# Kernel tuning notes

Measured on AMD Instinct MI355X. Metric: run time of the kernel, lower is better.

The kernel has to match this reference:

```python
import jax, jax.numpy as jnp
import numpy as np

# Module constants (from init_kwargs): 2D domain, m=[1024,1024], omega=[0,1,0,1]
PAD = 2
M0, M1 = 1024, 1024
OMEGA_LO = np.array([0.0, 0.0], dtype=np.float32)   # omega[0::2]
H = np.array([1.0 / 1024.0, 1.0 / 1024.0], dtype=np.float32)  # (omega_hi-omega_lo)/m
N_POINTS = 2097152


def _b0(j, xi):
    # Cubic B-spline basis pieces, exactly as SplineInter.b0
    if j == 1:
        return (2 + xi) * (2 + xi) * (2 + xi)
    elif j == 2:
        return -(3 * xi + 6) * (xi * xi) + 4
    elif j == 3:
        return (3 * xi - 6) * (xi * xi) + 4
    elif j == 4:
        return (2 - xi) * (2 - xi) * (2 - xi)


def _basis(t):
    # t: [N] fractional part; returns [N,4] weights for offsets j=-1,0,1,2
    # matches b0(3 - j, t - j)
    return jnp.stack([_b0(3 - j, t - j) for j in range(-1, 3)], axis=-1)


def setup_inputs() -> dict:
    key = jax.random.key(0)
    k1, k2 = jax.random.split(key)
    # query points in physical domain [0,1)^2 -> normalized coords in [-0.5, 1023.5)
    x = jax.random.uniform(k1, (N_POINTS, 2), dtype=jnp.float32)
    # padded spline coefficient grid: (M0+2*PAD, M1+2*PAD)
    coeffs = 0.1 * jax.random.normal(k2, (M0 + 2 * PAD, M1 + 2 * PAD), dtype=jnp.float32)
    return {"x": x, "coeffs": coeffs}


def reference(x, coeffs):
    x = x.reshape(-1, 2)
    # normalize to grid coords
    xn = (x - jnp.asarray(OMEGA_LO)) / jnp.asarray(H) - 0.5  # [N,2]
    m = jnp.array([M0, M1], dtype=xn.dtype)
    valid = jnp.all((xn > -2) & (xn < m), axis=1)            # [N]
    P = jnp.floor(xn).astype(jnp.int32)                      # [N,2]
    t = xn - P                                               # fractional part [N,2]

    i1 = M1 + 2 * PAD  # row stride of padded coeff grid
    p = i1 * (PAD + P[:, 0]) + (PAD + P[:, 1])               # [N] base flat index

    w0 = _basis(t[:, 0])  # [N,4]
    w1 = _basis(t[:, 1])  # [N,4]

    js = jnp.arange(-1, 3, dtype=jnp.int32)
    idx = p[:, None, None] + js[:, None] * i1 + js[None, :]  # [N,4,4]
    cflat = coeffs.reshape(-1)
    safe_idx = jnp.clip(idx, 0, cflat.shape[0] - 1)
    vals = cflat[safe_idx]                                   # [N,4,4] gathered stencil

    out = jnp.einsum('nij,ni,nj->n', vals, w0, w1)
    out = jnp.where(valid, out, 0.0)
    return out[:, None]  # [N,1]
```

## Files before the change

### kernel.cpp

```cpp
#include <hip/hip_runtime.h>


#define I1 1028
#define TOTAL (1028 * 1028)
#define NQR 257
#define QELEMS (NQR * I1)

typedef float f4u __attribute__((ext_vector_type(4), aligned(4)));

__device__ __forceinline__ void basis4(float t, float w[4]) {
    float a = 1.0f - t;
    w[0] = a * a * a;
    w[1] = (3.0f * t - 6.0f) * (t * t) + 4.0f;
    float xi = t - 1.0f;
    w[2] = -(3.0f * xi + 6.0f) * (xi * xi) + 4.0f;
    w[3] = t * t * t;
}

struct PointSetup {
    int base;
    int r0, c0;
    bool valid;
    bool qinterior;
    float w0[4], w1[4];
};

__device__ __forceinline__ PointSetup setup_point(float px, float py) {
    PointSetup ps;
    float xn0 = px * 1024.0f - 0.5f;
    float xn1 = py * 1024.0f - 0.5f;

    ps.valid = (xn0 > -2.0f) && (xn0 < 1024.0f) &&
               (xn1 > -2.0f) && (xn1 < 1024.0f);

    float P0f = floorf(xn0);
    float P1f = floorf(xn1);
    int P0 = (int)P0f;
    int P1 = (int)P1f;
    float t0 = xn0 - P0f;
    float t1 = xn1 - P1f;

    basis4(t0, ps.w0);
    basis4(t1, ps.w1);

    ps.base = I1 * (2 + P0) + (2 + P1);
    ps.r0 = P0 + 1;
    ps.c0 = P1 + 1;
    ps.qinterior = (ps.r0 >= 0) && (ps.r0 <= 1023) &&
                   (ps.c0 >= 0) && (ps.c0 + 3 <= 1027);
    return ps;
}

__device__ __forceinline__ float eval_slow(const float* __restrict__ coeffs,
                                           const PointSetup& ps) {
    float acc = 0.0f;
#pragma unroll
    for (int j = 0; j < 4; ++j) {
        int r = ps.base + (j - 1) * I1 - 1;
        float s = 0.0f;
#pragma unroll
        for (int k = 0; k < 4; ++k) {
            int idx = r + k;
            idx = min(max(idx, 0), TOTAL - 1);
            s = fmaf(coeffs[idx], ps.w1[k], s);
        }
        acc = fmaf(s, ps.w0[j], acc);
    }
    return acc;
}

__device__ __forceinline__ void shifted_w8(const float w0[4], int s, float W[8]) {
#pragma unroll
    for (int t = 0; t < 8; ++t) {
        float v = 0.0f;
        if (t - 0 >= 0 && t - 0 < 4) v = (s == 0) ? w0[t - 0] : v;
        if (t - 1 >= 0 && t - 1 < 4) v = (s == 1) ? w0[t - 1] : v;
        if (t - 2 >= 0 && t - 2 < 4) v = (s == 2) ? w0[t - 2] : v;
        if (t - 3 >= 0 && t - 3 < 4) v = (s == 3) ? w0[t - 3] : v;
        W[t] = v;
    }
}

__device__ __forceinline__ float reduce_quad(const float4 A[4], const float4 B[4],
                                             const float W[8], const float w1[4]) {
    float acc = 0.0f;
#pragma unroll
    for (int k = 0; k < 4; ++k) {
        float sk = fmaf(A[k].x, W[0],
                   fmaf(A[k].y, W[1],
                   fmaf(A[k].z, W[2],
                   fmaf(A[k].w, W[3],
                   fmaf(B[k].x, W[4],
                   fmaf(B[k].y, W[5],
                   fmaf(B[k].z, W[6],
                        B[k].w * W[7])))))));
        acc = fmaf(sk, w1[k], acc);
    }
    return acc;
}


__global__ __launch_bounds__(256) void quadpack_kernel(
    const float* __restrict__ coeffs, float4* __restrict__ Q)
{
    int i = blockIdx.x * blockDim.x + threadIdx.x;
    if (i >= QELEMS) return;
    int qr = i / I1;
    int c  = i - qr * I1;
    int r  = 4 * qr;
    float4 v;
    v.x = coeffs[(r + 0) * I1 + c];
    v.y = coeffs[(r + 1) * I1 + c];
    v.z = coeffs[(r + 2) * I1 + c];
    v.w = coeffs[(r + 3) * I1 + c];
    Q[i] = v;
}


__global__ __launch_bounds__(256) void eval_quad_kernel(
    const float* __restrict__ x,
    const float* __restrict__ coeffs,
    const float4* __restrict__ Q,
    float* __restrict__ out, int n)
{
    int g = blockIdx.x * blockDim.x + threadIdx.x;
    int i0 = 2 * g;
    if (i0 >= n) return;

    if (i0 + 1 < n) {
        float4 two = reinterpret_cast<const float4*>(x)[g];
        PointSetup psA = setup_point(two.x, two.y);
        PointSetup psB = setup_point(two.z, two.w);

        float accA, accB;
        if (psA.qinterior && psB.qinterior) {
            int sA = psA.r0 & 3, sB = psB.r0 & 3;
            const float4* qA = Q + (psA.r0 >> 2) * I1 + psA.c0;
            const float4* qB = Q + (psB.r0 >> 2) * I1 + psB.c0;
            float4 A0[4], A1[4], B0[4], B1[4];
#pragma unroll
            for (int k = 0; k < 4; ++k) {
                A0[k] = qA[k];
                B0[k] = qB[k];
            }
#pragma unroll
            for (int k = 0; k < 4; ++k) {
                A1[k] = qA[I1 + k];
                B1[k] = qB[I1 + k];
            }
            float WA[8], WB[8];
            shifted_w8(psA.w0, sA, WA);
            shifted_w8(psB.w0, sB, WB);
            accA = reduce_quad(A0, A1, WA, psA.w1);
            accB = reduce_quad(B0, B1, WB, psB.w1);
        } else {
            accA = eval_slow(coeffs, psA);
            accB = eval_slow(coeffs, psB);
        }

        float2 o;
        o.x = psA.valid ? accA : 0.0f;
        o.y = psB.valid ? accB : 0.0f;
        reinterpret_cast<float2*>(out)[g] = o;
    } else {
        float px = x[2 * i0], py = x[2 * i0 + 1];
        PointSetup ps = setup_point(px, py);
        float acc = eval_slow(coeffs, ps);
        out[i0] = ps.valid ? acc : 0.0f;
    }
}


__global__ __launch_bounds__(256) void spline_interp_kernel(
    const float* __restrict__ x,
    const float* __restrict__ coeffs,
    float* __restrict__ out,
    int n, int half)
{
    int i = blockIdx.x * blockDim.x + threadIdx.x;
    if (i >= half) return;
    int i2 = i + half;

    float2 xyA = reinterpret_cast<const float2*>(x)[i];
    float2 xyB = reinterpret_cast<const float2*>(x)[i2];

    PointSetup psA = setup_point(xyA.x, xyA.y);
    PointSetup psB = setup_point(xyB.x, xyB.y);

    float accA, accB;
    bool interiorA = (psA.base - I1 - 1 >= 0) && (psA.base + 2 * I1 + 2 <= TOTAL - 1);
    bool interiorB = (psB.base - I1 - 1 >= 0) && (psB.base + 2 * I1 + 2 <= TOTAL - 1);
    if (interiorA && interiorB) {
        f4u vA[4], vB[4];
#pragma unroll
        for (int j = 0; j < 4; ++j) {
            vA[j] = *reinterpret_cast<const f4u*>(coeffs + psA.base + (j - 1) * I1 - 1);
            vB[j] = *reinterpret_cast<const f4u*>(coeffs + psB.base + (j - 1) * I1 - 1);
        }
        float a0 = 0.0f, a1 = 0.0f;
#pragma unroll
        for (int j = 0; j < 4; ++j) {
            float s0 = fmaf(vA[j].x, psA.w1[0], fmaf(vA[j].y, psA.w1[1],
                       fmaf(vA[j].z, psA.w1[2], vA[j].w * psA.w1[3])));
            a0 = fmaf(s0, psA.w0[j], a0);
            float s1 = fmaf(vB[j].x, psB.w1[0], fmaf(vB[j].y, psB.w1[1],
                       fmaf(vB[j].z, psB.w1[2], vB[j].w * psB.w1[3])));
            a1 = fmaf(s1, psB.w0[j], a1);
        }
        accA = a0; accB = a1;
    } else {
        accA = eval_slow(coeffs, psA);
        accB = eval_slow(coeffs, psB);
    }

    out[i]  = psA.valid ? accA : 0.0f;
    out[i2] = psB.valid ? accB : 0.0f;
}


extern "C" void kernel_launch(void* const* d_in, const int* in_sizes, int n_in,
                              void* d_out, int out_size, void* d_ws, size_t ws_size,
                              hipStream_t stream) {
    const float* x = (const float*)d_in[0];
    const float* coeffs = (const float*)d_in[1];
    float* out = (float*)d_out;

    int n = in_sizes[0] / 2;

    size_t o_q  = 0;
    size_t need = (size_t)QELEMS * 16;

    if (ws_size >= need) {
        float4* Q = (float4*)((char*)d_ws + o_q);

        int gpack = (QELEMS + 255) / 256;
        quadpack_kernel<<<gpack, 256, 0, stream>>>(coeffs, Q);

        int pairs = (n + 1) / 2;
        int geval = (pairs + 255) / 256;
        eval_quad_kernel<<<geval, 256, 0, stream>>>(x, coeffs, Q, out, n);
    } else {
        int half = n / 2;
        int block = 256;
        int grid = (half + block - 1) / block;
        spline_interp_kernel<<<grid, block, 0, stream>>>(x, coeffs, out, n, half);
    }
}
```

Before: 107.0 us.

## Pack four row-phase-shifted float4 copies so each point reads one 4x4 stencil

Replaces the single 4-row-packed coefficient table with four copies, each starting at a different row offset. Each point then loads four float4 values (one per column) holding exactly its four stencil rows, instead of eight float4 loads across two packed rows plus shifted-weight selection. This halves per-point gather traffic and removes the weight-shifting ALU work. In exchange the pack kernel writes four times as much data (about 17 MB) and needs a larger workspace.

```diff
diff --git a/kernel.cpp b/kernel.cpp
--- a/kernel.cpp
+++ b/kernel.cpp
@@ -3,8 +3,10 @@
 
 #define I1 1028
 #define TOTAL (1028 * 1028)
-#define NQR 257
-#define QELEMS (NQR * I1)
+#define NQI 257
+#define COPY_ELEMS (NQI * I1)
+#define NCOPIES 4
+#define QTOT (NCOPIES * COPY_ELEMS)
 
 typedef float f4u __attribute__((ext_vector_type(4), aligned(4)));
 
@@ -46,8 +48,8 @@
     ps.base = I1 * (2 + P0) + (2 + P1);
     ps.r0 = P0 + 1;
     ps.c0 = P1 + 1;
-    ps.qinterior = (ps.r0 >= 0) && (ps.r0 <= 1023) &&
-                   (ps.c0 >= 0) && (ps.c0 + 3 <= 1027);
+    ps.qinterior = (ps.r0 >= 0) && (ps.r0 <= 1024) &&
+                   (ps.c0 >= 0) && (ps.c0 <= 1024);
     return ps;
 }
 
@@ -69,55 +71,44 @@
     return acc;
 }
 
-__device__ __forceinline__ void shifted_w8(const float w0[4], int s, float W[8]) {
-#pragma unroll
-    for (int t = 0; t < 8; ++t) {
-        float v = 0.0f;
-        if (t - 0 >= 0 && t - 0 < 4) v = (s == 0) ? w0[t - 0] : v;
-        if (t - 1 >= 0 && t - 1 < 4) v = (s == 1) ? w0[t - 1] : v;
-        if (t - 2 >= 0 && t - 2 < 4) v = (s == 2) ? w0[t - 2] : v;
-        if (t - 3 >= 0 && t - 3 < 4) v = (s == 3) ? w0[t - 3] : v;
-        W[t] = v;
-    }
-}
-
-__device__ __forceinline__ float reduce_quad(const float4 A[4], const float4 B[4],
-                                             const float W[8], const float w1[4]) {
+__device__ __forceinline__ float reduce_phase(const float4 v[4], const PointSetup& ps) {
     float acc = 0.0f;
 #pragma unroll
     for (int k = 0; k < 4; ++k) {
-        float sk = fmaf(A[k].x, W[0],
-                   fmaf(A[k].y, W[1],
-                   fmaf(A[k].z, W[2],
-                   fmaf(A[k].w, W[3],
-                   fmaf(B[k].x, W[4],
-                   fmaf(B[k].y, W[5],
-                   fmaf(B[k].z, W[6],
-                        B[k].w * W[7])))))));
-        acc = fmaf(sk, w1[k], acc);
+        float col = fmaf(v[k].x, ps.w0[0],
+                    fmaf(v[k].y, ps.w0[1],
+                    fmaf(v[k].z, ps.w0[2],
+                         v[k].w * ps.w0[3])));
+        acc = fmaf(col, ps.w1[k], acc);
     }
     return acc;
 }
 
 
-__global__ __launch_bounds__(256) void quadpack_kernel(
+__global__ __launch_bounds__(256) void phasepack_kernel(
     const float* __restrict__ coeffs, float4* __restrict__ Q)
 {
-    int i = blockIdx.x * blockDim.x + threadIdx.x;
-    if (i >= QELEMS) return;
-    int qr = i / I1;
-    int c  = i - qr * I1;
-    int r  = 4 * qr;
+    int idx = blockIdx.x * blockDim.x + threadIdx.x;
+    if (idx >= QTOT) return;
+    int p   = idx / COPY_ELEMS;
+    int rem = idx - p * COPY_ELEMS;
+    int i   = rem / I1;
+    int c   = rem - i * I1;
+    int r   = 4 * i + p;
+    int r0 = min(r,     1027);
+    int r1 = min(r + 1, 1027);
+    int r2 = min(r + 2, 1027);
+    int r3 = min(r + 3, 1027);
     float4 v;
-    v.x = coeffs[(r + 0) * I1 + c];
-    v.y = coeffs[(r + 1) * I1 + c];
-    v.z = coeffs[(r + 2) * I1 + c];
-    v.w = coeffs[(r + 3) * I1 + c];
-    Q[i] = v;
-}
-
-
-__global__ __launch_bounds__(256) void eval_quad_kernel(
+    v.x = coeffs[r0 * I1 + c];
+    v.y = coeffs[r1 * I1 + c];
+    v.z = coeffs[r2 * I1 + c];
+    v.w = coeffs[r3 * I1 + c];
+    Q[idx] = v;
+}
+
+
+__global__ __launch_bounds__(256) void eval_phase_kernel(
     const float* __restrict__ x,
     const float* __restrict__ coeffs,
     const float4* __restrict__ Q,
@@ -134,25 +125,18 @@
 
         float accA, accB;
         if (psA.qinterior && psB.qinterior) {
-            int sA = psA.r0 & 3, sB = psB.r0 & 3;
-            const float4* qA = Q + (psA.r0 >> 2) * I1 + psA.c0;
-            const float4* qB = Q + (psB.r0 >> 2) * I1 + psB.c0;
-            float4 A0[4], A1[4], B0[4], B1[4];
+            const float4* qA = Q + (psA.r0 & 3) * COPY_ELEMS
+                                 + (psA.r0 >> 2) * I1 + psA.c0;
+            const float4* qB = Q + (psB.r0 & 3) * COPY_ELEMS
+                                 + (psB.r0 >> 2) * I1 + psB.c0;
+            float4 vA[4], vB[4];
 #pragma unroll
             for (int k = 0; k < 4; ++k) {
-                A0[k] = qA[k];
-                B0[k] = qB[k];
+                vA[k] = qA[k];
+                vB[k] = qB[k];
             }
-#pragma unroll
-            for (int k = 0; k < 4; ++k) {
-                A1[k] = qA[I1 + k];
-                B1[k] = qB[I1 + k];
-            }
-            float WA[8], WB[8];
-            shifted_w8(psA.w0, sA, WA);
-            shifted_w8(psB.w0, sB, WB);
-            accA = reduce_quad(A0, A1, WA, psA.w1);
-            accB = reduce_quad(B0, B1, WB, psB.w1);
+            accA = reduce_phase(vA, psA);
+            accB = reduce_phase(vB, psB);
         } else {
             accA = eval_slow(coeffs, psA);
             accB = eval_slow(coeffs, psB);
@@ -227,18 +211,17 @@
 
     int n = in_sizes[0] / 2;
 
-    size_t o_q  = 0;
-    size_t need = (size_t)QELEMS * 16;
+    size_t need = (size_t)QTOT * 16;
 
     if (ws_size >= need) {
-        float4* Q = (float4*)((char*)d_ws + o_q);
-
-        int gpack = (QELEMS + 255) / 256;
-        quadpack_kernel<<<gpack, 256, 0, stream>>>(coeffs, Q);
+        float4* Q = (float4*)d_ws;
+
+        int gpack = (QTOT + 255) / 256;
+        phasepack_kernel<<<gpack, 256, 0, stream>>>(coeffs, Q);
 
         int pairs = (n + 1) / 2;
         int geval = (pairs + 255) / 256;
-        eval_quad_kernel<<<geval, 256, 0, stream>>>(x, coeffs, Q, out, n);
+        eval_phase_kernel<<<geval, 256, 0, stream>>>(x, coeffs, Q, out, n);
     } else {
         int half = n / 2;
         int block = 256;
```

New measurement: 111.1 us. 3.9% more time.
